# Optimization experiments

Hardware: AMD Instinct MI355X
Metric: run time of the kernel (lower is better)

The kernel has to match this reference:

```python
import jax, jax.numpy as jnp
import numpy as np

N, E, F, H, OUT = 50000, 500000, 128, 128, 768

def _lin(x, W, b):
    return x @ W + b

def _layernorm(x, g, b, eps=1e-5):
    mu = jnp.mean(x, axis=-1, keepdims=True)
    var = jnp.var(x, axis=-1, keepdims=True)
    return (x - mu) * jax.lax.rsqrt(var + eps) * g + b

def _edge_softmax(alpha, dst, n_nodes):
    # softmax over incoming edges per destination node, per channel
    amax = jax.ops.segment_max(alpha, dst, num_segments=n_nodes)
    ex = jnp.exp(alpha - amax[dst])
    denom = jax.ops.segment_sum(ex, dst, num_segments=n_nodes)
    return ex / denom[dst]

def setup_inputs() -> dict:
    key = jax.random.key(0)
    ks = jax.random.split(key, 24)
    def w(k, i, o):
        return (jax.random.normal(k, (i, o), jnp.float32) / np.float32(np.sqrt(i)))
    inp = {
        'kind': jax.random.normal(ks[0], (N, F), jnp.float32),
        'edge_h': jax.random.normal(ks[1], (E, F), jnp.float32),
        'src': jax.random.randint(ks[2], (E,), 0, N, jnp.int32),
        'dst': jax.random.randint(ks[3], (E,), 0, N, jnp.int32),
        'KW': w(ks[4], 2 * F, H), 'Kb': jnp.zeros((H,), jnp.float32),
        'VW': w(ks[5], 2 * F, H), 'Vb': jnp.zeros((H,), jnp.float32),
        'QW': w(ks[6], F, H), 'Qb': jnp.zeros((H,), jnp.float32),
        'WW': w(ks[7], F + H, H), 'Wb': jnp.zeros((H,), jnp.float32),
        'K2W': w(ks[8], 3 * F, H), 'K2b': jnp.zeros((H,), jnp.float32),
        'V2W': w(ks[9], 3 * F, H), 'V2b': jnp.zeros((H,), jnp.float32),
        'Q2W': w(ks[10], 2 * F, H), 'Q2b': jnp.zeros((H,), jnp.float32),
        'W2W': w(ks[11], 2 * F + H, OUT), 'W2b': jnp.zeros((OUT,), jnp.float32),
        'ln1_g': jnp.ones((H,), jnp.float32), 'ln1_b': jnp.zeros((H,), jnp.float32),
        'ln2_g': jnp.ones((OUT,), jnp.float32), 'ln2_b': jnp.zeros((OUT,), jnp.float32),
        'gate_w': w(ks[12], OUT, 1), 'gate_b': jnp.zeros((1,), jnp.float32),
    }
    return inp

def reference(kind, edge_h, src, dst, KW, Kb, VW, Vb, QW, Qb, WW, Wb,
              K2W, K2b, V2W, V2b, Q2W, Q2b, W2W, W2b,
              ln1_g, ln1_b, ln2_g, ln2_b, gate_w, gate_b):
    n_nodes = kind.shape[0]
    src_kind = kind[src]                               # [E,F] gather
    # --- layer 1 ---
    Q = _lin(kind, QW, Qb)                             # [N,H]
    ek_in = jnp.concatenate([src_kind, edge_h], axis=1)  # [E,2F]
    eK = _lin(ek_in, KW, Kb)                           # [E,H]
    eV = _lin(ek_in, VW, Vb)                           # [E,H]
    alpha = _edge_softmax(Q[dst] * eK, dst, n_nodes)   # [E,H]
    h_n = jax.ops.segment_sum(alpha * eV, dst, num_segments=n_nodes)  # [N,H]
    h = _layernorm(_lin(jnp.concatenate([h_n, kind], axis=1), WW, Wb), ln1_g, ln1_b)
    # --- layer 2 ---
    Q2 = _lin(jnp.concatenate([kind, h], axis=1), Q2W, Q2b)            # [N,H]
    ek2_in = jnp.concatenate([src_kind, edge_h, h[src]], axis=1)       # [E,3F]
    eK2 = _lin(ek2_in, K2W, K2b)
    eV2 = _lin(ek2_in, V2W, V2b)
    alpha2 = _edge_softmax(Q2[dst] * eK2, dst, n_nodes)
    h_n1 = jax.ops.segment_sum(alpha2 * eV2, dst, num_segments=n_nodes)
    h1 = _layernorm(_lin(jnp.concatenate([h_n1, h, kind], axis=1), W2W, W2b), ln2_g, ln2_b)  # [N,768]
    # --- global attention pooling (single graph) ---
    gate = jax.nn.softmax(_lin(h1, gate_w, gate_b), axis=0)  # [N,1]
    graph_vec = jnp.sum(gate * h1, axis=0, keepdims=True)    # [1,768]
    return graph_vec
```

## Files before the change

kernel.cpp:

```cpp
#include <hip/hip_runtime.h>

typedef float f32x4 __attribute__((ext_vector_type(4)));
typedef short bf16x8 __attribute__((ext_vector_type(8)));
typedef unsigned short ushort8 __attribute__((ext_vector_type(8)));

__device__ __forceinline__ float bf2f(unsigned short u) {
    return __uint_as_float(((unsigned int)u) << 16);
}
__device__ __forceinline__ unsigned short f2bf(float f) {
    unsigned int u = __float_as_uint(f);
    u += 0x7FFFu + ((u >> 16) & 1u);
    return (unsigned short)(u >> 16);
}
__device__ __forceinline__ float pld(const void* p, long i, bool isbf) {
    return isbf ? bf2f(((const unsigned short*)p)[i]) : ((const float*)p)[i];
}

#define ASYNC16(gp, lp)                                                        \
    __builtin_amdgcn_global_load_lds(                                          \
        (__attribute__((address_space(1))) unsigned int*)(gp),                 \
        (__attribute__((address_space(3))) unsigned int*)(lp), 16, 0, 0)

__global__ void probe_kernel(const unsigned int* __restrict__ w, int* __restrict__ flag) {
    if (threadIdx.x == 0 && blockIdx.x == 0)
        *flag = (w[0] == 0x3F803F80u) ? 1 : 0;
}

__global__ __launch_bounds__(256) void cvt_kernel(
    const void* __restrict__ src_, unsigned short* __restrict__ dst_,
    const int* __restrict__ flag, long n8)
{
    const bool isbf = (*flag != 0);
    long stride = (long)gridDim.x * blockDim.x;
    for (long i = (long)blockIdx.x * blockDim.x + threadIdx.x; i < n8; i += stride) {
        if (isbf) {
            ((ushort8*)dst_)[i] = ((const ushort8*)src_)[i];
        } else {
            const float4* s = (const float4*)src_ + i * 2;
            float4 a = s[0], b = s[1];
            ushort8 r;
            r[0] = f2bf(a.x); r[1] = f2bf(a.y); r[2] = f2bf(a.z); r[3] = f2bf(a.w);
            r[4] = f2bf(b.x); r[5] = f2bf(b.y); r[6] = f2bf(b.z); r[7] = f2bf(b.w);
            ((ushort8*)dst_)[i] = r;
        }
    }
}

template <int WM, int WN>
__global__ __launch_bounds__(256) void gemm_kernel(
    const unsigned short* __restrict__ seg0, const unsigned short* __restrict__ seg1,
    const unsigned short* __restrict__ seg2,
    const int* __restrict__ gi0, const int* __restrict__ gi1, const int* __restrict__ gi2,
    const unsigned short* __restrict__ Bt, const float* __restrict__ bias,
    int M, int K, int Nout,
    float* __restrict__ outF, unsigned short* __restrict__ outB)
{
    constexpr int BM = WM * 64, BN = WN * 64;
    constexpr int AI = BM / 64;
    constexpr int BI = BN / 64;
    constexpr int PB = BN + 8;
    constexpr int STAGE = (BM + BN) * 32 * 2;
    constexpr int PANEL = 16 * PB * 4;
    constexpr int SH = STAGE > PANEL ? STAGE : PANEL;
    __shared__ __attribute__((aligned(16))) char shraw[SH];
    unsigned short* lA = (unsigned short*)shraw;
    unsigned short* lB = lA + BM * 32;

    const int tid  = threadIdx.x;
    const int wave = tid >> 6, lane = tid & 63;
    const int wm = wave / WN, wn = wave % WN;

    const int rsub = tid >> 2;
    const int csel = (tid & 3) ^ ((tid >> 3) & 3);

    const unsigned short* aptr0[AI];
    const unsigned short* aptr1[AI];
    const unsigned short* aptr2[AI];
#pragma unroll
    for (int i = 0; i < AI; ++i) {
        int gr = blockIdx.x * BM + rsub + 64 * i;
        if (gr >= M) gr = M - 1;
        aptr0[i] = seg0 + (long)(gi0 ? gi0[gr] : gr) * 128;
        aptr1[i] = seg1 ? seg1 + (long)(gi1 ? gi1[gr] : gr) * 128 : aptr0[i];
        aptr2[i] = seg2 ? seg2 + (long)(gi2 ? gi2[gr] : gr) * 128 : aptr0[i];
    }
    const unsigned short* bptr[BI];
#pragma unroll
    for (int i = 0; i < BI; ++i) {
        int bn = blockIdx.y * BN + rsub + 64 * i;
        bptr[i] = Bt + (long)bn * K;
    }

    f32x4 acc[4][4];
#pragma unroll
    for (int a = 0; a < 4; ++a)
#pragma unroll
        for (int b = 0; b < 4; ++b) acc[a][b] = (f32x4)(0.0f);

    const int q = lane >> 4, mrow = lane & 15;

    for (int kk = 0; kk < K; kk += 32) {
        __syncthreads();
        const int s = kk >> 7, koff = kk & 127;
#pragma unroll
        for (int i = 0; i < AI; ++i) {
            const unsigned short* ap = (s == 0) ? aptr0[i] : ((s == 1) ? aptr1[i] : aptr2[i]);
            ASYNC16(ap + koff + csel * 8, &lA[tid * 8 + i * 2048]);
        }
#pragma unroll
        for (int i = 0; i < BI; ++i) {
            ASYNC16(bptr[i] + kk + csel * 8, &lB[tid * 8 + i * 2048]);
        }
        __syncthreads();

        bf16x8 af[4], bfv[4];
#pragma unroll
        for (int t = 0; t < 4; ++t) {
            int r = wm * 64 + t * 16 + mrow;
            af[t] = *(const bf16x8*)&lA[r * 32 + ((q ^ ((r >> 1) & 3)) * 8)];
        }
#pragma unroll
        for (int t = 0; t < 4; ++t) {
            int r = wn * 64 + t * 16 + mrow;
            bfv[t] = *(const bf16x8*)&lB[r * 32 + ((q ^ ((r >> 1) & 3)) * 8)];
        }
#pragma unroll
        for (int tm = 0; tm < 4; ++tm)
#pragma unroll
            for (int tn = 0; tn < 4; ++tn)
                acc[tm][tn] = __builtin_amdgcn_mfma_f32_16x16x32_bf16(af[tm], bfv[tn], acc[tm][tn], 0, 0, 0);
    }

    float bv[4];
#pragma unroll
    for (int tn = 0; tn < 4; ++tn) {
        int col = blockIdx.y * BN + wn * 64 + tn * 16 + mrow;
        bv[tn] = bias ? bias[col] : 0.0f;
    }
    float*          pf = (float*)shraw;
    unsigned short* pb = (unsigned short*)shraw;

#pragma unroll
    for (int p = 0; p < BM / 16; ++p) {
        const int pw = p >> 2;
        const int tm = p & 3;
        __syncthreads();
        if (wm == pw) {
#pragma unroll
            for (int tn = 0; tn < 4; ++tn) {
                int cl = wn * 64 + tn * 16 + mrow;
#pragma unroll
                for (int r = 0; r < 4; ++r) {
                    int pr = q * 4 + r;
                    float v = acc[tm][tn][r] + bv[tn];
                    if (outF) pf[pr * PB + cl] = v;
                    else      pb[pr * PB + cl] = f2bf(v);
                }
            }
        }
        __syncthreads();
        const int rowbase = blockIdx.x * BM + p * 16;
        if (outF) {
            constexpr int CPR = BN / 4;
            for (int c = tid; c < 16 * CPR; c += 256) {
                int pr = c / CPR, co = (c - pr * CPR) * 4;
                int grow = rowbase + pr;
                if (grow < M)
                    *(float4*)(outF + (long)grow * Nout + blockIdx.y * BN + co) =
                        *(const float4*)(pf + pr * PB + co);
            }
        } else {
            constexpr int CPR = BN / 8;
            for (int c = tid; c < 16 * CPR; c += 256) {
                int pr = c / CPR, co = (c - pr * CPR) * 8;
                int grow = rowbase + pr;
                if (grow < M)
                    *(ushort8*)(outB + (long)grow * Nout + blockIdx.y * BN + co) =
                        *(const ushort8*)(pb + pr * PB + co);
            }
        }
    }
}

__global__ void hist_kernel(const int* __restrict__ dst, int* __restrict__ counts, int E) {
    int e = blockIdx.x * blockDim.x + threadIdx.x;
    if (e < E) atomicAdd(&counts[dst[e]], 1);
}

__global__ __launch_bounds__(1024) void scan_kernel(const int* __restrict__ counts,
                                                    int* __restrict__ indptr,
                                                    int* __restrict__ wp, int N) {
    __shared__ int wsum[16];
    __shared__ int carry;
    int tid = threadIdx.x;
    int wave = tid >> 6, lane = tid & 63;
    if (tid == 0) carry = 0;
    __syncthreads();
    for (int base = 0; base < N; base += 1024) {
        int c0 = carry;
        int i = base + tid;
        int v = (i < N) ? counts[i] : 0;
        int s = v;
#pragma unroll
        for (int off = 1; off < 64; off <<= 1) {
            int t = __shfl_up(s, off, 64);
            if (lane >= off) s += t;
        }
        if (lane == 63) wsum[wave] = s;
        __syncthreads();
        if (wave == 0 && lane < 16) {
            int w = wsum[lane];
#pragma unroll
            for (int off = 1; off < 16; off <<= 1) {
                int t = __shfl_up(w, off, 64);
                if (lane >= off) w += t;
            }
            wsum[lane] = w;
        }
        __syncthreads();
        int woff = wave ? wsum[wave - 1] : 0;
        if (i < N) { int ex = c0 + woff + s - v; indptr[i] = ex; wp[i] = ex; }
        __syncthreads();
        if (tid == 0) carry = c0 + wsum[15];
        __syncthreads();
    }
    if (tid == 0) indptr[N] = carry;
}

__global__ void scatter_kernel(const int* __restrict__ dst, int* __restrict__ wp,
                               int* __restrict__ eidx, int E) {
    int e = blockIdx.x * blockDim.x + threadIdx.x;
    if (e < E) {
        int slot = atomicAdd(&wp[dst[e]], 1);
        eidx[slot] = e;
    }
}

__global__ __launch_bounds__(256) void edge_softmax_kernel(
    const int* __restrict__ indptr, const int* __restrict__ eidx,
    const int* __restrict__ src,
    const float* __restrict__ Q, const unsigned short* __restrict__ ekv,
    const unsigned short* __restrict__ nkv,
    unsigned short* __restrict__ hn, int N)
{
    int wave = threadIdx.x >> 6, lane = threadIdx.x & 63;
    int n = blockIdx.x * 4 + wave;
    if (n >= N) return;
    int beg = indptr[n], end = indptr[n + 1];
    int c = lane << 1;
    float q0 = Q[(long)n * 128 + c], q1 = Q[(long)n * 128 + c + 1];
    float m0 = -3.4e38f, m1 = -3.4e38f, d0 = 0.f, d1 = 0.f, a0 = 0.f, a1 = 0.f;
    for (int i = beg; i < end; ++i) {
        int e = eidx[i];
        int sv = src[e];
        const unsigned short* er = ekv + (long)e * 256 + c;
        const unsigned short* nr = nkv + (long)sv * 256 + c;
        unsigned int kk = *(const unsigned int*)er;
        unsigned int vv = *(const unsigned int*)(er + 128);
        unsigned int nk = *(const unsigned int*)nr;
        unsigned int nv = *(const unsigned int*)(nr + 128);
        float k0 = bf2f((unsigned short)kk) + bf2f((unsigned short)nk);
        float k1 = bf2f((unsigned short)(kk >> 16)) + bf2f((unsigned short)(nk >> 16));
        float v0 = bf2f((unsigned short)vv) + bf2f((unsigned short)nv);
        float v1 = bf2f((unsigned short)(vv >> 16)) + bf2f((unsigned short)(nv >> 16));
        float s0 = q0 * k0, s1 = q1 * k1;
        float nm0 = fmaxf(m0, s0), nm1 = fmaxf(m1, s1);
        float e00 = __expf(m0 - nm0), e01 = __expf(s0 - nm0);
        float e10 = __expf(m1 - nm1), e11 = __expf(s1 - nm1);
        d0 = d0 * e00 + e01; a0 = a0 * e00 + e01 * v0; m0 = nm0;
        d1 = d1 * e10 + e11; a1 = a1 * e10 + e11 * v1; m1 = nm1;
    }
    float r0 = (end > beg) ? a0 / d0 : 0.f;
    float r1 = (end > beg) ? a1 / d1 : 0.f;
    unsigned int pk = (unsigned int)f2bf(r0) | ((unsigned int)f2bf(r1) << 16);
    *(unsigned int*)(hn + (long)n * 128 + c) = pk;
}

__global__ __launch_bounds__(256) void ln128_kernel(
    const float* __restrict__ x, const float* __restrict__ g,
    const float* __restrict__ b, unsigned short* __restrict__ y, int N)
{
    int wave = threadIdx.x >> 6, lane = threadIdx.x & 63;
    int n = blockIdx.x * 4 + wave;
    if (n >= N) return;
    int c = lane << 1;
    float2 v = *(const float2*)(x + (long)n * 128 + c);
    float s = v.x + v.y;
#pragma unroll
    for (int o = 1; o < 64; o <<= 1) s += __shfl_xor(s, o, 64);
    float mu = s * (1.f / 128.f);
    float dx0 = v.x - mu, dx1 = v.y - mu;
    float sq = dx0 * dx0 + dx1 * dx1;
#pragma unroll
    for (int o = 1; o < 64; o <<= 1) sq += __shfl_xor(sq, o, 64);
    float rs = rsqrtf(sq * (1.f / 128.f) + 1e-5f);
    float y0 = dx0 * rs * g[c] + b[c];
    float y1 = dx1 * rs * g[c + 1] + b[c + 1];
    unsigned int pk = (unsigned int)f2bf(y0) | ((unsigned int)f2bf(y1) << 16);
    *(unsigned int*)(y + (long)n * 128 + c) = pk;
}

__global__ __launch_bounds__(256) void ln768_kernel(
    const float* __restrict__ x, const float* __restrict__ g,
    const float* __restrict__ b, const float* __restrict__ gw,
    const float* __restrict__ gbias,
    unsigned short* __restrict__ y, float* __restrict__ gout, int N)
{
    __shared__ float red[4];
    __shared__ float red2[4];
    int n = blockIdx.x;
    int tid = threadIdx.x;
    int wave = tid >> 6, lane = tid & 63;
    const float* xr = x + (long)n * 768;
    float v0 = xr[tid], v1 = xr[tid + 256], v2 = xr[tid + 512];
    float s = v0 + v1 + v2;
#pragma unroll
    for (int o = 1; o < 64; o <<= 1) s += __shfl_xor(s, o, 64);
    if (lane == 0) red[wave] = s;
    __syncthreads();
    float mu = (red[0] + red[1] + red[2] + red[3]) * (1.f / 768.f);
    float d0 = v0 - mu, d1 = v1 - mu, d2 = v2 - mu;
    float sq = d0 * d0 + d1 * d1 + d2 * d2;
#pragma unroll
    for (int o = 1; o < 64; o <<= 1) sq += __shfl_xor(sq, o, 64);
    __syncthreads();
    if (lane == 0) red[wave] = sq;
    __syncthreads();
    float rs = rsqrtf((red[0] + red[1] + red[2] + red[3]) * (1.f / 768.f) + 1e-5f);
    float y0 = d0 * rs * g[tid]       + b[tid];
    float y1 = d1 * rs * g[tid + 256] + b[tid + 256];
    float y2 = d2 * rs * g[tid + 512] + b[tid + 512];
    unsigned short* yr = y + (long)n * 768;
    yr[tid]       = f2bf(y0);
    yr[tid + 256] = f2bf(y1);
    yr[tid + 512] = f2bf(y2);
    float dot = y0 * gw[tid] + y1 * gw[tid + 256] + y2 * gw[tid + 512];
#pragma unroll
    for (int o = 1; o < 64; o <<= 1) dot += __shfl_xor(dot, o, 64);
    if (lane == 0) red2[wave] = dot;
    __syncthreads();
    if (tid == 0) gout[n] = red2[0] + red2[1] + red2[2] + red2[3] + gbias[0];
}

__global__ __launch_bounds__(256) void reduce_max_kernel(
    const float* __restrict__ gv, unsigned int* __restrict__ gmax, int N)
{
    __shared__ float red[4];
    int tid = threadIdx.x, wave = tid >> 6, lane = tid & 63;
    float m = -3.4e38f;
    for (int i = blockIdx.x * 256 + tid; i < N; i += gridDim.x * 256)
        m = fmaxf(m, gv[i]);
#pragma unroll
    for (int o = 1; o < 64; o <<= 1) m = fmaxf(m, __shfl_xor(m, o, 64));
    if (lane == 0) red[wave] = m;
    __syncthreads();
    if (tid == 0) {
        m = fmaxf(fmaxf(red[0], red[1]), fmaxf(red[2], red[3]));
        unsigned int u = __float_as_uint(m);
        u = (u & 0x80000000u) ? ~u : (u | 0x80000000u);
        atomicMax(gmax, u);
    }
}

__global__ __launch_bounds__(256) void gate_acc_kernel(
    const unsigned short* __restrict__ h1, const float* __restrict__ gv,
    const unsigned int* __restrict__ gmax_u, float* __restrict__ num,
    float* __restrict__ Z, int N)
{
    unsigned int mu = *gmax_u;
    float gm = (mu & 0x80000000u) ? __uint_as_float(mu & 0x7FFFFFFFu) : __uint_as_float(~mu);
    int tid = threadIdx.x;
    float a0 = 0.f, a1 = 0.f, a2 = 0.f, z = 0.f;
    for (int n = blockIdx.x; n < N; n += gridDim.x) {
        float ex = __expf(gv[n] - gm);
        const unsigned short* hr = h1 + (long)n * 768;
        a0 += ex * bf2f(hr[tid]);
        a1 += ex * bf2f(hr[tid + 256]);
        a2 += ex * bf2f(hr[tid + 512]);
        z += ex;
    }
    atomicAdd(num + tid, a0);
    atomicAdd(num + tid + 256, a1);
    atomicAdd(num + tid + 512, a2);
    if (tid == 0) atomicAdd(Z, z);
}

__global__ void finalize_kernel(const float* __restrict__ num, const float* __restrict__ Z,
                                void* __restrict__ out, const int* __restrict__ flag) {
    int i = blockIdx.x * blockDim.x + threadIdx.x;
    if (i < 768) {
        float v = num[i] / *Z;
        if (*flag) ((unsigned short*)out)[i] = f2bf(v);
        else       ((float*)out)[i] = v;
    }
}

__global__ void transpose_kernel(
    const void* QW, const void* KW, const void* VW, const void* WW,
    const void* Q2W, const void* K2W, const void* V2W, const void* W2W,
    unsigned short* tQ, unsigned short* tNKV1, unsigned short* tEKV1,
    unsigned short* tW, unsigned short* tQ2,
    unsigned short* tNKV2, unsigned short* tEKV2, unsigned short* tW2,
    const int* __restrict__ flag)
{
    const bool isbf = (*flag != 0);
    const int mode = blockIdx.y;
    unsigned short* dstp; int Kd, Nr;
    switch (mode) {
        case 0:  dstp = tQ;    Kd = 128; Nr = 128; break;
        case 1:  dstp = tNKV1; Kd = 128; Nr = 256; break;
        case 2:  dstp = tEKV1; Kd = 128; Nr = 256; break;
        case 3:  dstp = tW;    Kd = 256; Nr = 128; break;
        case 4:  dstp = tQ2;   Kd = 256; Nr = 128; break;
        case 5:  dstp = tNKV2; Kd = 256; Nr = 256; break;
        case 6:  dstp = tEKV2; Kd = 128; Nr = 256; break;
        default: dstp = tW2;   Kd = 384; Nr = 768; break;
    }
    int total = Kd * Nr;
    for (int idx = blockIdx.x * blockDim.x + threadIdx.x; idx < total;
         idx += gridDim.x * blockDim.x) {
        int n = idx / Kd, k = idx - n * Kd;
        float v;
        switch (mode) {
            case 0:  v = pld(QW,  (long)k * 128 + n, isbf); break;
            case 1:  v = pld(n < 128 ? KW : VW, (long)k * 128 + (n & 127), isbf); break;
            case 2:  v = pld(n < 128 ? KW : VW, (long)(k + 128) * 128 + (n & 127), isbf); break;
            case 3:  v = pld(WW,  (long)k * 128 + n, isbf); break;
            case 4:  v = pld(Q2W, (long)k * 128 + n, isbf); break;
            case 5:  v = pld(n < 128 ? K2W : V2W,
                             (long)(k < 128 ? k : k + 128) * 128 + (n & 127), isbf); break;
            case 6:  v = pld(n < 128 ? K2W : V2W, (long)(k + 128) * 128 + (n & 127), isbf); break;
            default: v = pld(W2W, (long)k * 768 + n, isbf); break;
        }
        dstp[(long)n * Kd + k] = f2bf(v);
    }
}

__global__ void init_kernel(
    const int* __restrict__ flag, int* counts, float* num, float* Z, unsigned int* gmax,
    const void* Qb, const void* Kb, const void* Vb, const void* Wb,
    const void* Q2b, const void* K2b, const void* V2b, const void* W2b,
    const void* l1g, const void* l1b, const void* l2g, const void* l2b,
    const void* gw, const void* gb,
    float* bQ, float* bKV, float* bW, float* bQ2, float* bKV2, float* bW2,
    float* f1g, float* f1b, float* f2g, float* f2b, float* fgw, float* fgb, int N)
{
    const bool isbf = (*flag != 0);
    int i = blockIdx.x * blockDim.x + threadIdx.x;
    if (i < N) counts[i] = 0;
    if (i < 768) {
        num[i] = 0.f;
        bW2[i] = pld(W2b, i, isbf);
        f2g[i] = pld(l2g, i, isbf); f2b[i] = pld(l2b, i, isbf);
        fgw[i] = pld(gw, i, isbf);
    }
    if (i < 128) {
        bQ[i] = pld(Qb, i, isbf); bW[i] = pld(Wb, i, isbf); bQ2[i] = pld(Q2b, i, isbf);
        bKV[i] = pld(Kb, i, isbf);  bKV[i + 128] = pld(Vb, i, isbf);
        bKV2[i] = pld(K2b, i, isbf); bKV2[i + 128] = pld(V2b, i, isbf);
        f1g[i] = pld(l1g, i, isbf); f1b[i] = pld(l1b, i, isbf);
    }
    if (i == 0) { *Z = 0.f; *gmax = 0u; fgb[0] = pld(gb, 0, isbf); }
}

extern "C" void kernel_launch(void* const* d_in, const int* in_sizes, int n_in,
                              void* d_out, int out_size, void* d_ws, size_t ws_size,
                              hipStream_t stream)
{
    const void* kind   = d_in[0];
    const void* edge_h = d_in[1];
    const int* src = (const int*)d_in[2];
    const int* dst = (const int*)d_in[3];
    const void* KW  = d_in[4];  const void* Kb  = d_in[5];
    const void* VW  = d_in[6];  const void* Vb  = d_in[7];
    const void* QW  = d_in[8];  const void* Qb  = d_in[9];
    const void* WW  = d_in[10]; const void* Wb  = d_in[11];
    const void* K2W = d_in[12]; const void* K2b = d_in[13];
    const void* V2W = d_in[14]; const void* V2b = d_in[15];
    const void* Q2W = d_in[16]; const void* Q2b = d_in[17];
    const void* W2W = d_in[18]; const void* W2b = d_in[19];
    const void* ln1g = d_in[20]; const void* ln1b = d_in[21];
    const void* ln2g = d_in[22]; const void* ln2b = d_in[23];
    const void* gw  = d_in[24]; const void* gb  = d_in[25];

    const int N = in_sizes[0] / 128;
    const int E = in_sizes[2];

    char* wsp = (char*)d_ws;
    auto alloc = [&](size_t bytes) -> char* {
        char* p = wsp;
        wsp += (bytes + 255) & ~(size_t)255;
        return p;
    };
    unsigned short* tQ    = (unsigned short*)alloc(128 * 128 * 2);
    unsigned short* tNKV1 = (unsigned short*)alloc(256 * 128 * 2);
    unsigned short* tEKV1 = (unsigned short*)alloc(256 * 128 * 2);
    unsigned short* tW    = (unsigned short*)alloc(128 * 256 * 2);
    unsigned short* tQ2   = (unsigned short*)alloc(128 * 256 * 2);
    unsigned short* tNKV2 = (unsigned short*)alloc(256 * 256 * 2);
    unsigned short* tEKV2 = (unsigned short*)alloc(256 * 128 * 2);
    unsigned short* tW2   = (unsigned short*)alloc(768 * 384 * 2);
    float* bQ   = (float*)alloc(128 * 4);
    float* bKV  = (float*)alloc(256 * 4);
    float* bW   = (float*)alloc(128 * 4);
    float* bQ2  = (float*)alloc(128 * 4);
    float* bKV2 = (float*)alloc(256 * 4);
    float* bW2  = (float*)alloc(768 * 4);
    float* f1g = (float*)alloc(128 * 4);
    float* f1b = (float*)alloc(128 * 4);
    float* f2g = (float*)alloc(768 * 4);
    float* f2b = (float*)alloc(768 * 4);
    float* fgw = (float*)alloc(768 * 4);
    float* fgb = (float*)alloc(256);
    int*   flag = (int*)alloc(256);
    unsigned short* kindB = (unsigned short*)alloc((size_t)N * 128 * 2);
    unsigned short* edgeB = (unsigned short*)alloc((size_t)E * 128 * 2);
    float* Qbuf = (float*)alloc((size_t)N * 128 * 4);
    unsigned short* nkv1 = (unsigned short*)alloc((size_t)N * 256 * 2);
    unsigned short* nkv2 = (unsigned short*)alloc((size_t)N * 256 * 2);

    size_t h1off = ((size_t)N * 768 * 4 + 255) & ~(size_t)255;
    size_t bigsz = (size_t)E * 512;
    size_t need  = h1off + (size_t)N * 768 * 2;
    if (need > bigsz) bigsz = need;
    char* big = alloc(bigsz);
    unsigned short* ekv   = (unsigned short*)big;
    float*          preh1 = (float*)big;
    unsigned short* h1    = (unsigned short*)(big + h1off);

    unsigned short* hn = (unsigned short*)alloc((size_t)N * 128 * 2);
    unsigned short* h  = (unsigned short*)alloc((size_t)N * 128 * 2);
    int* counts = (int*)alloc((size_t)N * 4);
    int* indptr = (int*)alloc((size_t)(N + 1) * 4);
    int* wp     = (int*)alloc((size_t)N * 4);
    int* eidx   = (int*)alloc((size_t)E * 4);
    float* g    = (float*)alloc((size_t)N * 4);
    unsigned int* gmaxp = (unsigned int*)alloc(256);
    float* Zp   = (float*)alloc(256);
    float* nump = (float*)alloc(768 * 4);

    probe_kernel<<<1, 64, 0, stream>>>((const unsigned int*)ln1g, flag);
    init_kernel<<<(N + 255) / 256, 256, 0, stream>>>(
        flag, counts, nump, Zp, gmaxp, Qb, Kb, Vb, Wb, Q2b, K2b, V2b, W2b,
        ln1g, ln1b, ln2g, ln2b, gw, gb,
        bQ, bKV, bW, bQ2, bKV2, bW2, f1g, f1b, f2g, f2b, fgw, fgb, N);
    transpose_kernel<<<dim3(64, 8), 256, 0, stream>>>(
        QW, KW, VW, WW, Q2W, K2W, V2W, W2W,
        tQ, tNKV1, tEKV1, tW, tQ2, tNKV2, tEKV2, tW2, flag);
    cvt_kernel<<<512, 256, 0, stream>>>(kind, kindB, flag, (long)N * 16);
    cvt_kernel<<<1024, 256, 0, stream>>>(edge_h, edgeB, flag, (long)E * 16);
    hist_kernel<<<(E + 255) / 256, 256, 0, stream>>>(dst, counts, E);
    scan_kernel<<<1, 1024, 0, stream>>>(counts, indptr, wp, N);
    scatter_kernel<<<(E + 255) / 256, 256, 0, stream>>>(dst, wp, eidx, E);

    gemm_kernel<2, 2><<<dim3((N + 127) / 128, 1), 256, 0, stream>>>(
        kindB, nullptr, nullptr, nullptr, nullptr, nullptr,
        tQ, bQ, N, 128, 128, Qbuf, nullptr);
    gemm_kernel<2, 2><<<dim3((N + 127) / 128, 2), 256, 0, stream>>>(
        kindB, nullptr, nullptr, nullptr, nullptr, nullptr,
        tNKV1, bKV, N, 128, 256, nullptr, nkv1);
    gemm_kernel<1, 4><<<dim3((E + 63) / 64, 1), 256, 0, stream>>>(
        edgeB, nullptr, nullptr, nullptr, nullptr, nullptr,
        tEKV1, nullptr, E, 128, 256, nullptr, ekv);
    edge_softmax_kernel<<<(N + 3) / 4, 256, 0, stream>>>(
        indptr, eidx, src, Qbuf, ekv, nkv1, hn, N);
    gemm_kernel<2, 2><<<dim3((N + 127) / 128, 1), 256, 0, stream>>>(
        hn, kindB, nullptr, nullptr, nullptr, nullptr,
        tW, bW, N, 256, 128, Qbuf, nullptr);
    ln128_kernel<<<(N + 3) / 4, 256, 0, stream>>>(Qbuf, f1g, f1b, h, N);

    gemm_kernel<2, 2><<<dim3((N + 127) / 128, 1), 256, 0, stream>>>(
        kindB, h, nullptr, nullptr, nullptr, nullptr,
        tQ2, bQ2, N, 256, 128, Qbuf, nullptr);
    gemm_kernel<2, 2><<<dim3((N + 127) / 128, 2), 256, 0, stream>>>(
        kindB, h, nullptr, nullptr, nullptr, nullptr,
        tNKV2, bKV2, N, 256, 256, nullptr, nkv2);
    gemm_kernel<1, 4><<<dim3((E + 63) / 64, 1), 256, 0, stream>>>(
        edgeB, nullptr, nullptr, nullptr, nullptr, nullptr,
        tEKV2, nullptr, E, 128, 256, nullptr, ekv);
    edge_softmax_kernel<<<(N + 3) / 4, 256, 0, stream>>>(
        indptr, eidx, src, Qbuf, ekv, nkv2, hn, N);
    gemm_kernel<1, 4><<<dim3((N + 63) / 64, 3), 256, 0, stream>>>(
        hn, h, kindB, nullptr, nullptr, nullptr,
        tW2, bW2, N, 384, 768, preh1, nullptr);
    ln768_kernel<<<N, 256, 0, stream>>>(preh1, f2g, f2b, fgw, fgb, h1, g, N);

    reduce_max_kernel<<<256, 256, 0, stream>>>(g, gmaxp, N);
    gate_acc_kernel<<<256, 256, 0, stream>>>(h1, g, gmaxp, nump, Zp, N);
    finalize_kernel<<<3, 256, 0, stream>>>(nump, Zp, d_out, flag);
}
```

Before: 1.363 ms.

## Fuse edge K/V GEMMs, permute edges by destination, convert edge features in-kernel

Both layers' edge-side K/V projections now run as one GEMM over edge_h with a concatenated 512-column weight. Rows are gathered through the dst-sorted edge index, so outputs come out in CSR order, and the fp32-to-bf16 conversion happens inside the A-tile load. The softmax kernel then reads edge K/V contiguously by CSR position and uses a pre-permuted src array, which removes the eidx/src double indirection and the separate edge_h conversion pass. The cost is a doubled ekv buffer (E×1024 bytes), a gathered non-async A load in the GEMM, and the second-layer edge K/V being computed before it is needed.

```diff
diff --git a/kernel.cpp b/kernel.cpp
--- a/kernel.cpp
+++ b/kernel.cpp
@@ -46,11 +46,12 @@
     }
 }
 
-template <int WM, int WN>
+template <int WM, int WN, bool CVTA = false>
 __global__ __launch_bounds__(256) void gemm_kernel(
-    const unsigned short* __restrict__ seg0, const unsigned short* __restrict__ seg1,
+    const void* __restrict__ seg0v, const unsigned short* __restrict__ seg1,
     const unsigned short* __restrict__ seg2,
     const int* __restrict__ gi0, const int* __restrict__ gi1, const int* __restrict__ gi2,
+    const int* __restrict__ aflag,
     const unsigned short* __restrict__ Bt, const float* __restrict__ bias,
     int M, int K, int Nout,
     float* __restrict__ outF, unsigned short* __restrict__ outB)
@@ -73,16 +74,30 @@
     const int rsub = tid >> 2;
     const int csel = (tid & 3) ^ ((tid >> 3) & 3);
 
+    const unsigned short* seg0 = (const unsigned short*)seg0v;
     const unsigned short* aptr0[AI];
     const unsigned short* aptr1[AI];
     const unsigned short* aptr2[AI];
-#pragma unroll
-    for (int i = 0; i < AI; ++i) {
-        int gr = blockIdx.x * BM + rsub + 64 * i;
-        if (gr >= M) gr = M - 1;
-        aptr0[i] = seg0 + (long)(gi0 ? gi0[gr] : gr) * 128;
-        aptr1[i] = seg1 ? seg1 + (long)(gi1 ? gi1[gr] : gr) * 128 : aptr0[i];
-        aptr2[i] = seg2 ? seg2 + (long)(gi2 ? gi2[gr] : gr) * 128 : aptr0[i];
+    const char* arowc[AI];
+    bool af32 = false;
+    if constexpr (CVTA) {
+        af32 = (*aflag == 0);
+        const int rb = af32 ? 512 : 256;
+#pragma unroll
+        for (int i = 0; i < AI; ++i) {
+            int gr = blockIdx.x * BM + rsub + 64 * i;
+            if (gr >= M) gr = M - 1;
+            arowc[i] = (const char*)seg0v + (long)(gi0 ? gi0[gr] : gr) * rb;
+        }
+    } else {
+#pragma unroll
+        for (int i = 0; i < AI; ++i) {
+            int gr = blockIdx.x * BM + rsub + 64 * i;
+            if (gr >= M) gr = M - 1;
+            aptr0[i] = seg0 + (long)(gi0 ? gi0[gr] : gr) * 128;
+            aptr1[i] = seg1 ? seg1 + (long)(gi1 ? gi1[gr] : gr) * 128 : aptr0[i];
+            aptr2[i] = seg2 ? seg2 + (long)(gi2 ? gi2[gr] : gr) * 128 : aptr0[i];
+        }
     }
     const unsigned short* bptr[BI];
 #pragma unroll
@@ -101,11 +116,28 @@
 
     for (int kk = 0; kk < K; kk += 32) {
         __syncthreads();
-        const int s = kk >> 7, koff = kk & 127;
-#pragma unroll
-        for (int i = 0; i < AI; ++i) {
-            const unsigned short* ap = (s == 0) ? aptr0[i] : ((s == 1) ? aptr1[i] : aptr2[i]);
-            ASYNC16(ap + koff + csel * 8, &lA[tid * 8 + i * 2048]);
+        if constexpr (CVTA) {
+            const int eo = kk + csel * 8;
+#pragma unroll
+            for (int i = 0; i < AI; ++i) {
+                ushort8 r;
+                if (af32) {
+                    const float4* s = (const float4*)((const float*)arowc[i] + eo);
+                    float4 a = s[0], b = s[1];
+                    r[0] = f2bf(a.x); r[1] = f2bf(a.y); r[2] = f2bf(a.z); r[3] = f2bf(a.w);
+                    r[4] = f2bf(b.x); r[5] = f2bf(b.y); r[6] = f2bf(b.z); r[7] = f2bf(b.w);
+                } else {
+                    r = *(const ushort8*)((const unsigned short*)arowc[i] + eo);
+                }
+                *(ushort8*)&lA[tid * 8 + i * 2048] = r;
+            }
+        } else {
+            const int s = kk >> 7, koff = kk & 127;
+#pragma unroll
+            for (int i = 0; i < AI; ++i) {
+                const unsigned short* ap = (s == 0) ? aptr0[i] : ((s == 1) ? aptr1[i] : aptr2[i]);
+                ASYNC16(ap + koff + csel * 8, &lA[tid * 8 + i * 2048]);
+            }
         }
 #pragma unroll
         for (int i = 0; i < BI; ++i) {
@@ -227,21 +259,22 @@
     if (tid == 0) indptr[N] = carry;
 }
 
-__global__ void scatter_kernel(const int* __restrict__ dst, int* __restrict__ wp,
-                               int* __restrict__ eidx, int E) {
+__global__ void scatter_kernel(const int* __restrict__ dst, const int* __restrict__ src,
+                               int* __restrict__ wp,
+                               int* __restrict__ eidx, int* __restrict__ srcs, int E) {
     int e = blockIdx.x * blockDim.x + threadIdx.x;
     if (e < E) {
         int slot = atomicAdd(&wp[dst[e]], 1);
         eidx[slot] = e;
+        srcs[slot] = src[e];
     }
 }
 
 __global__ __launch_bounds__(256) void edge_softmax_kernel(
-    const int* __restrict__ indptr, const int* __restrict__ eidx,
-    const int* __restrict__ src,
+    const int* __restrict__ indptr, const int* __restrict__ srcs,
     const float* __restrict__ Q, const unsigned short* __restrict__ ekv,
     const unsigned short* __restrict__ nkv,
-    unsigned short* __restrict__ hn, int N)
+    unsigned short* __restrict__ hn, int N, int off)
 {
     int wave = threadIdx.x >> 6, lane = threadIdx.x & 63;
     int n = blockIdx.x * 4 + wave;
@@ -251,9 +284,8 @@
     float q0 = Q[(long)n * 128 + c], q1 = Q[(long)n * 128 + c + 1];
     float m0 = -3.4e38f, m1 = -3.4e38f, d0 = 0.f, d1 = 0.f, a0 = 0.f, a1 = 0.f;
     for (int i = beg; i < end; ++i) {
-        int e = eidx[i];
-        int sv = src[e];
-        const unsigned short* er = ekv + (long)e * 256 + c;
+        int sv = srcs[i];
+        const unsigned short* er = ekv + (long)i * 512 + off + c;
         const unsigned short* nr = nkv + (long)sv * 256 + c;
         unsigned int kk = *(const unsigned int*)er;
         unsigned int vv = *(const unsigned int*)(er + 128);
@@ -398,23 +430,23 @@
 __global__ void transpose_kernel(
     const void* QW, const void* KW, const void* VW, const void* WW,
     const void* Q2W, const void* K2W, const void* V2W, const void* W2W,
-    unsigned short* tQ, unsigned short* tNKV1, unsigned short* tEKV1,
+    unsigned short* tQ, unsigned short* tNKV1, unsigned short* tEKV,
     unsigned short* tW, unsigned short* tQ2,
-    unsigned short* tNKV2, unsigned short* tEKV2, unsigned short* tW2,
+    unsigned short* tNKV2, unsigned short* tW2,
     const int* __restrict__ flag)
 {
     const bool isbf = (*flag != 0);
     const int mode = blockIdx.y;
     unsigned short* dstp; int Kd, Nr;
     switch (mode) {
-        case 0:  dstp = tQ;    Kd = 128; Nr = 128; break;
-        case 1:  dstp = tNKV1; Kd = 128; Nr = 256; break;
-        case 2:  dstp = tEKV1; Kd = 128; Nr = 256; break;
-        case 3:  dstp = tW;    Kd = 256; Nr = 128; break;
-        case 4:  dstp = tQ2;   Kd = 256; Nr = 128; break;
-        case 5:  dstp = tNKV2; Kd = 256; Nr = 256; break;
-        case 6:  dstp = tEKV2; Kd = 128; Nr = 256; break;
-        default: dstp = tW2;   Kd = 384; Nr = 768; break;
+        case 0:  dstp = tQ;              Kd = 128; Nr = 128; break;
+        case 1:  dstp = tNKV1;           Kd = 128; Nr = 256; break;
+        case 2:  dstp = tEKV;            Kd = 128; Nr = 256; break;
+        case 3:  dstp = tW;              Kd = 256; Nr = 128; break;
+        case 4:  dstp = tQ2;             Kd = 256; Nr = 128; break;
+        case 5:  dstp = tNKV2;           Kd = 256; Nr = 256; break;
+        case 6:  dstp = tEKV + 256*128;  Kd = 128; Nr = 256; break;
+        default: dstp = tW2;             Kd = 384; Nr = 768; break;
     }
     int total = Kd * Nr;
     for (int idx = blockIdx.x * blockDim.x + threadIdx.x; idx < total;
@@ -494,11 +526,10 @@
     };
     unsigned short* tQ    = (unsigned short*)alloc(128 * 128 * 2);
     unsigned short* tNKV1 = (unsigned short*)alloc(256 * 128 * 2);
-    unsigned short* tEKV1 = (unsigned short*)alloc(256 * 128 * 2);
+    unsigned short* tEKV  = (unsigned short*)alloc(512 * 128 * 2);
     unsigned short* tW    = (unsigned short*)alloc(128 * 256 * 2);
     unsigned short* tQ2   = (unsigned short*)alloc(128 * 256 * 2);
     unsigned short* tNKV2 = (unsigned short*)alloc(256 * 256 * 2);
-    unsigned short* tEKV2 = (unsigned short*)alloc(256 * 128 * 2);
     unsigned short* tW2   = (unsigned short*)alloc(768 * 384 * 2);
     float* bQ   = (float*)alloc(128 * 4);
     float* bKV  = (float*)alloc(256 * 4);
@@ -514,13 +545,12 @@
     float* fgb = (float*)alloc(256);
     int*   flag = (int*)alloc(256);
     unsigned short* kindB = (unsigned short*)alloc((size_t)N * 128 * 2);
-    unsigned short* edgeB = (unsigned short*)alloc((size_t)E * 128 * 2);
     float* Qbuf = (float*)alloc((size_t)N * 128 * 4);
     unsigned short* nkv1 = (unsigned short*)alloc((size_t)N * 256 * 2);
     unsigned short* nkv2 = (unsigned short*)alloc((size_t)N * 256 * 2);
 
     size_t h1off = ((size_t)N * 768 * 4 + 255) & ~(size_t)255;
-    size_t bigsz = (size_t)E * 512;
+    size_t bigsz = (size_t)E * 1024;
     size_t need  = h1off + (size_t)N * 768 * 2;
     if (need > bigsz) bigsz = need;
     char* big = alloc(bigsz);
@@ -534,6 +564,7 @@
     int* indptr = (int*)alloc((size_t)(N + 1) * 4);
     int* wp     = (int*)alloc((size_t)N * 4);
     int* eidx   = (int*)alloc((size_t)E * 4);
+    int* srcs   = (int*)alloc((size_t)E * 4);
     float* g    = (float*)alloc((size_t)N * 4);
     unsigned int* gmaxp = (unsigned int*)alloc(256);
     float* Zp   = (float*)alloc(256);
@@ -546,42 +577,39 @@
         bQ, bKV, bW, bQ2, bKV2, bW2, f1g, f1b, f2g, f2b, fgw, fgb, N);
     transpose_kernel<<<dim3(64, 8), 256, 0, stream>>>(
         QW, KW, VW, WW, Q2W, K2W, V2W, W2W,
-        tQ, tNKV1, tEKV1, tW, tQ2, tNKV2, tEKV2, tW2, flag);
+        tQ, tNKV1, tEKV, tW, tQ2, tNKV2, tW2, flag);
     cvt_kernel<<<512, 256, 0, stream>>>(kind, kindB, flag, (long)N * 16);
-    cvt_kernel<<<1024, 256, 0, stream>>>(edge_h, edgeB, flag, (long)E * 16);
     hist_kernel<<<(E + 255) / 256, 256, 0, stream>>>(dst, counts, E);
     scan_kernel<<<1, 1024, 0, stream>>>(counts, indptr, wp, N);
-    scatter_kernel<<<(E + 255) / 256, 256, 0, stream>>>(dst, wp, eidx, E);
+    scatter_kernel<<<(E + 255) / 256, 256, 0, stream>>>(dst, src, wp, eidx, srcs, E);
+
+    gemm_kernel<1, 4, true><<<dim3((E + 63) / 64, 2), 256, 0, stream>>>(
+        edge_h, nullptr, nullptr, eidx, nullptr, nullptr, flag,
+        tEKV, nullptr, E, 128, 512, nullptr, ekv);
 
     gemm_kernel<2, 2><<<dim3((N + 127) / 128, 1), 256, 0, stream>>>(
-        kindB, nullptr, nullptr, nullptr, nullptr, nullptr,
+        kindB, nullptr, nullptr, nullptr, nullptr, nullptr, nullptr,
         tQ, bQ, N, 128, 128, Qbuf, nullptr);
     gemm_kernel<2, 2><<<dim3((N + 127) / 128, 2), 256, 0, stream>>>(
-        kindB, nullptr, nullptr, nullptr, nullptr, nullptr,
+        kindB, nullptr, nullptr, nullptr, nullptr, nullptr, nullptr,
         tNKV1, bKV, N, 128, 256, nullptr, nkv1);
-    gemm_kernel<1, 4><<<dim3((E + 63) / 64, 1), 256, 0, stream>>>(
-        edgeB, nullptr, nullptr, nullptr, nullptr, nullptr,
-        tEKV1, nullptr, E, 128, 256, nullptr, ekv);
     edge_softmax_kernel<<<(N + 3) / 4, 256, 0, stream>>>(
-        indptr, eidx, src, Qbuf, ekv, nkv1, hn, N);
+        indptr, srcs, Qbuf, ekv, nkv1, hn, N, 0);
     gemm_kernel<2, 2><<<dim3((N + 127) / 128, 1), 256, 0, stream>>>(
-        hn, kindB, nullptr, nullptr, nullptr, nullptr,
+        hn, kindB, nullptr, nullptr, nullptr, nullptr, nullptr,
         tW, bW, N, 256, 128, Qbuf, nullptr);
     ln128_kernel<<<(N + 3) / 4, 256, 0, stream>>>(Qbuf, f1g, f1b, h, N);
 
     gemm_kernel<2, 2><<<dim3((N + 127) / 128, 1), 256, 0, stream>>>(
-        kindB, h, nullptr, nullptr, nullptr, nullptr,
+        kindB, h, nullptr, nullptr, nullptr, nullptr, nullptr,
         tQ2, bQ2, N, 256, 128, Qbuf, nullptr);
     gemm_kernel<2, 2><<<dim3((N + 127) / 128, 2), 256, 0, stream>>>(
-        kindB, h, nullptr, nullptr, nullptr, nullptr,
+        kindB, h, nullptr, nullptr, nullptr, nullptr, nullptr,
         tNKV2, bKV2, N, 256, 256, nullptr, nkv2);
-    gemm_kernel<1, 4><<<dim3((E + 63) / 64, 1), 256, 0, stream>>>(
-        edgeB, nullptr, nullptr, nullptr, nullptr, nullptr,
-        tEKV2, nullptr, E, 128, 256, nullptr, ekv);
     edge_softmax_kernel<<<(N + 3) / 4, 256, 0, stream>>>(
-        indptr, eidx, src, Qbuf, ekv, nkv2, hn, N);
+        indptr, srcs, Qbuf, ekv, nkv2, hn, N, 256);
     gemm_kernel<1, 4><<<dim3((N + 63) / 64, 3), 256, 0, stream>>>(
-        hn, h, kindB, nullptr, nullptr, nullptr,
+        hn, h, kindB, nullptr, nullptr, nullptr, nullptr,
         tW2, bW2, N, 384, 768, preh1, nullptr);
     ln768_kernel<<<N, 256, 0, stream>>>(preh1, f2g, f2b, fgw, fgb, h1, g, N);
 
```

After: 1.268 ms. 7.0% less time.
